# Optimization experiments

Measured on AMD Instinct MI355X. Metric: run time of the kernel, lower is better.

Reference implementation:

```python
import jax, jax.numpy as jnp
import numpy as np

RADIUS = 0.2
NSAMPLE = 64


def _ball_query(xyz, new_xyz):
    """PointNet++-style ball query: first NSAMPLE point indices within RADIUS
    of each center; empty slots filled with the first found index.
    xyz: (B, N, 3), new_xyz: (B, P, 3) -> idx: (B, P, NSAMPLE) int32."""
    N = xyz.shape[1]
    # squared distances (B, P, N)
    d2 = jnp.sum((new_xyz[:, :, None, :] - xyz[:, None, :, :]) ** 2, axis=-1)
    # score = point index if inside ball else sentinel N; smallest NSAMPLE scores
    # give the first NSAMPLE in-ball indices in ascending order (CUDA order).
    scores = jnp.where(d2 < RADIUS * RADIUS, jnp.arange(N, dtype=jnp.int32), N)
    neg_vals, _ = jax.lax.top_k(-scores, NSAMPLE)
    idx = -neg_vals  # ascending smallest scores
    first = idx[..., :1]
    return jnp.where(idx < N, idx, first)


def setup_inputs() -> dict:
    key = jax.random.key(0)
    k1, k2, k3 = jax.random.split(key, 3)
    B, N, P, C = 4, 16384, 1024, 128
    xyz = jax.random.uniform(k1, (B, N, 3), dtype=jnp.float32)
    new_xyz = jax.random.uniform(k2, (B, P, 3), dtype=jnp.float32)
    features = jax.random.normal(k3, (B, C, N), dtype=jnp.float32)
    return {"xyz": xyz, "new_xyz": new_xyz, "features": features}


def reference(xyz, new_xyz, features):
    B, N, _ = xyz.shape
    idx0 = _ball_query(xyz, new_xyz)  # (B, P, S), returned as bq_idx
    # dedup: slots (other than slot 0) equal to the first index are the
    # padding fills -> redirect them to the shadow point at index N
    first = idx0[..., :1]
    dup = (idx0 == first).at[..., 0].set(False)
    idx = jnp.where(dup, N, idx0)

    # shadow xyz = 1e6, shadow feature = 0
    xyz_pad = jnp.concatenate([xyz, jnp.full((B, 1, 3), 1.0e6, xyz.dtype)], axis=1)
    grouped_xyz = jax.vmap(lambda p, i: p[i])(xyz_pad, idx)        # (B, P, S, 3)
    grouped_xyz = grouped_xyz.transpose(0, 3, 1, 2)                # (B, 3, P, S)
    grouped_xyz = grouped_xyz - new_xyz.transpose(0, 2, 1)[..., None]

    feats_pad = jnp.concatenate([features, jnp.zeros_like(features[:, :, :1])], axis=-1)
    grouped_feat = jax.vmap(lambda p, i: p[i])(feats_pad.transpose(0, 2, 1), idx)  # (B, P, S, C)
    grouped_feat = grouped_feat.transpose(0, 3, 1, 2)              # (B, C, P, S)

    # use_xyz=True: zero shadow coords, normalize by radius, concat
    xyz_feature = jnp.where(grouped_xyz > 1.0e5, 0.0, grouped_xyz) / RADIUS
    new_features = jnp.concatenate([xyz_feature, grouped_feat], axis=1)  # (B, 3+C, P, S)
    return new_features, grouped_xyz, idx0
```

## Files before the change

kernel.cpp:

```cpp
#include <hip/hip_runtime.h>
#include <cstdint>

#define BQ_B 4
#define BQ_N 16384
#define BQ_P 1024
#define BQ_C 128
#define NS   64
#define R2   0.04f

#define O1 ((size_t)BQ_B * 131 * BQ_P * NS)
#define O2 (O1 + (size_t)BQ_B * 3 * BQ_P * NS)

#define WS_T_BYTES ((size_t)BQ_B * BQ_N * BQ_C * 4)

__global__ __launch_bounds__(256) void transpose_kernel(
    const float* __restrict__ f, float* __restrict__ ft)
{
    const int bid = blockIdx.x;
    const int n0 = (bid & 255) * 64;
    const int c0 = ((bid >> 8) & 1) * 64;
    const int b  = bid >> 9;
    __shared__ float tile[64][65];

    const float* fb = f + ((size_t)b * BQ_C + c0) * BQ_N;
    #pragma unroll
    for (int k = 0; k < 16; ++k) {
        const int cc = k * 4 + (threadIdx.x >> 6);
        const int nn = threadIdx.x & 63;
        tile[cc][nn] = fb[(size_t)cc * BQ_N + n0 + nn];
    }
    __syncthreads();
    float* ob = ft + ((size_t)b * BQ_N + n0) * BQ_C + c0;
    #pragma unroll
    for (int k = 0; k < 16; ++k) {
        const int nn = k * 4 + (threadIdx.x >> 6);
        const int cc = threadIdx.x & 63;
        ob[(size_t)nn * BQ_C + cc] = tile[cc][nn];
    }
}

__global__ __launch_bounds__(512, 8) void query_gather_kernel(
    const float* __restrict__ xyz,
    const float* __restrict__ new_xyz,
    const float* __restrict__ ft,
    float* __restrict__ out)
{
#pragma clang fp contract(off)
    const int center = blockIdx.x;
    const int b = center >> 10;
    const int p = center & (BQ_P - 1);
    const int t = threadIdx.x;
    const int lane = t & 63;
    const int w = t >> 6;

    __shared__ unsigned long long smask[64];
    __shared__ int   sprefix[64];
    __shared__ int   s_total;
    __shared__ int   lds_idx[NS];
    __shared__ int   gidx_s[NS];
    __shared__ float tile[NS][BQ_C + 1];

    const float cx = new_xyz[center * 3 + 0];
    const float cy = new_xyz[center * 3 + 1];
    const float cz = new_xyz[center * 3 + 2];
    const float* xb = xyz + (size_t)b * BQ_N * 3;

    int total = 0;
    const unsigned long long lmask = (1ull << lane) - 1ull;

    for (int round = 0; round < 4; ++round) {
        const int rbase = round * 4096;
        #pragma unroll
        for (int k = 0; k < 8; ++k) {
            const int j = w * 8 + k;
            const int i = rbase + j * 64 + lane;
            const float dx = xb[i * 3 + 0] - cx;
            const float dy = xb[i * 3 + 1] - cy;
            const float dz = xb[i * 3 + 2] - cz;
            const float d2 = dx * dx + dy * dy + dz * dz;
            const unsigned long long m = __ballot(d2 < R2);
            if (lane == 0) smask[j] = m;
        }
        __syncthreads();

        if (w == 0) {
            const unsigned long long mm = smask[lane];
            const int cnt = (int)__popcll(mm);
            int x = cnt;
            #pragma unroll
            for (int d = 1; d < 64; d <<= 1) {
                const int y = __shfl_up(x, d, 64);
                if (lane >= d) x += y;
            }
            sprefix[lane] = total + (x - cnt);
            if (lane == 63) s_total = total + x;
        }
        __syncthreads();

        const int new_total = s_total;
        #pragma unroll
        for (int k = 0; k < 8; ++k) {
            const int j = w * 8 + k;
            const unsigned long long m = smask[j];
            const int baser = sprefix[j];
            if (baser < NS && ((m >> lane) & 1ull)) {
                const int r = baser + (int)__popcll(m & lmask);
                if (r < NS) lds_idx[r] = rbase + j * 64 + lane;
            }
        }
        total = new_total;
        if (new_total >= NS) break;
    }
    __syncthreads();

    if (t < NS) {
        const int tt = (total > NS) ? NS : total;
        const int first = (total > 0) ? lds_idx[0] : BQ_N;
        const int v = (t < tt) ? lds_idx[t] : BQ_N;
        const int idx0 = (t < tt) ? v : first;
        const int gidx = v;
        const bool real = gidx < BQ_N;
        gidx_s[t] = gidx;

        out[O2 + (size_t)center * NS + t] = (float)idx0;

        #pragma unroll
        for (int d = 0; d < 3; ++d) {
            const float c = (d == 0) ? cx : ((d == 1) ? cy : cz);
            const float pt = real ? xb[gidx * 3 + d] : 1000000.0f;
            const float g = pt - c;
            out[O1 + ((size_t)(b * 3 + d) * BQ_P + p) * NS + t] = g;
            const float xf = ((g > 100000.0f) ? 0.0f : g) / 0.2f;
            out[((size_t)(b * 131 + d) * BQ_P + p) * NS + t] = xf;
        }
    }
    __syncthreads();

    const float* fb = ft + (size_t)b * BQ_N * BQ_C;
    #pragma unroll
    for (int k = 0; k < 16; ++k) {
        const int s = k * 4 + (t >> 7);
        const int c = t & 127;
        const int gi = gidx_s[s];
        tile[s][c] = (gi < BQ_N) ? fb[(size_t)gi * BQ_C + c] : 0.0f;
    }
    __syncthreads();
    float* ob = out + ((size_t)(b * 131 + 3) * BQ_P + p) * NS;
    #pragma unroll
    for (int k = 0; k < 16; ++k) {
        const int c = k * 8 + (t >> 6);
        const int s = t & 63;
        ob[(size_t)c * (BQ_P * NS) + s] = tile[s][c];
    }
}

extern "C" void kernel_launch(void* const* d_in, const int* in_sizes, int n_in,
                              void* d_out, int out_size, void* d_ws, size_t ws_size,
                              hipStream_t stream) {
    const float* xyz      = (const float*)d_in[0];
    const float* new_xyz  = (const float*)d_in[1];
    const float* features = (const float*)d_in[2];
    float* out = (float*)d_out;
    float* ft  = (float*)d_ws;

    transpose_kernel<<<dim3(BQ_B * 2 * 256), dim3(256), 0, stream>>>(features, ft);
    query_gather_kernel<<<dim3(BQ_B * BQ_P), dim3(512), 0, stream>>>(xyz, new_xyz, ft, out);
}
```

Baseline: 234.6 us.

## Split ball query and feature gather into separate kernels with float4 gather

Splits the fused query+gather kernel into a ball-query kernel, which writes indices to workspace, and a separate row-gather kernel. The query block shrinks from 512 to 256 threads, with each wave scanning 16 chunks. The gather kernel uses float4 loads from the transposed features and float4 stores to the output. The aim is to free the heavy-LDS gather from the scan's occupancy limits and to vectorize memory access. The cost is an extra launch and an index round trip through global memory, and LDS column reads in the float4 store may hit bank conflicts.

```diff
diff --git a/kernel.cpp b/kernel.cpp
--- a/kernel.cpp
+++ b/kernel.cpp
@@ -39,10 +39,10 @@
     }
 }
 
-__global__ __launch_bounds__(512, 8) void query_gather_kernel(
+__global__ __launch_bounds__(256) void ballquery_kernel(
     const float* __restrict__ xyz,
     const float* __restrict__ new_xyz,
-    const float* __restrict__ ft,
+    int* __restrict__ wsIdx,
     float* __restrict__ out)
 {
 #pragma clang fp contract(off)
@@ -54,11 +54,9 @@
     const int w = t >> 6;
 
     __shared__ unsigned long long smask[64];
-    __shared__ int   sprefix[64];
-    __shared__ int   s_total;
-    __shared__ int   lds_idx[NS];
-    __shared__ int   gidx_s[NS];
-    __shared__ float tile[NS][BQ_C + 1];
+    __shared__ int sprefix[64];
+    __shared__ int s_total;
+    __shared__ int lds_idx[NS];
 
     const float cx = new_xyz[center * 3 + 0];
     const float cy = new_xyz[center * 3 + 1];
@@ -71,8 +69,8 @@
     for (int round = 0; round < 4; ++round) {
         const int rbase = round * 4096;
         #pragma unroll
-        for (int k = 0; k < 8; ++k) {
-            const int j = w * 8 + k;
+        for (int k = 0; k < 16; ++k) {
+            const int j = w * 16 + k;
             const int i = rbase + j * 64 + lane;
             const float dx = xb[i * 3 + 0] - cx;
             const float dy = xb[i * 3 + 1] - cy;
@@ -99,8 +97,8 @@
 
         const int new_total = s_total;
         #pragma unroll
-        for (int k = 0; k < 8; ++k) {
-            const int j = w * 8 + k;
+        for (int k = 0; k < 16; ++k) {
+            const int j = w * 16 + k;
             const unsigned long long m = smask[j];
             const int baser = sprefix[j];
             if (baser < NS && ((m >> lane) & 1ull)) {
@@ -118,39 +116,61 @@
         const int first = (total > 0) ? lds_idx[0] : BQ_N;
         const int v = (t < tt) ? lds_idx[t] : BQ_N;
         const int idx0 = (t < tt) ? v : first;
-        const int gidx = v;
-        const bool real = gidx < BQ_N;
-        gidx_s[t] = gidx;
+        const bool real = v < BQ_N;
 
+        wsIdx[(size_t)center * NS + t] = v;
         out[O2 + (size_t)center * NS + t] = (float)idx0;
 
         #pragma unroll
         for (int d = 0; d < 3; ++d) {
             const float c = (d == 0) ? cx : ((d == 1) ? cy : cz);
-            const float pt = real ? xb[gidx * 3 + d] : 1000000.0f;
+            const float pt = real ? xb[v * 3 + d] : 1000000.0f;
             const float g = pt - c;
             out[O1 + ((size_t)(b * 3 + d) * BQ_P + p) * NS + t] = g;
             const float xf = ((g > 100000.0f) ? 0.0f : g) / 0.2f;
             out[((size_t)(b * 131 + d) * BQ_P + p) * NS + t] = xf;
         }
     }
+}
+
+__global__ __launch_bounds__(256) void row_gather_kernel(
+    const float* __restrict__ ft,
+    const int* __restrict__ wsIdx,
+    float* __restrict__ out)
+{
+    const int center = blockIdx.x;
+    const int b = center >> 10;
+    const int p = center & (BQ_P - 1);
+    const int t = threadIdx.x;
+
+    __shared__ int   sg[NS];
+    __shared__ float tile[NS][BQ_C + 1];
+
+    if (t < NS) sg[t] = wsIdx[(size_t)center * NS + t];
     __syncthreads();
 
     const float* fb = ft + (size_t)b * BQ_N * BQ_C;
     #pragma unroll
-    for (int k = 0; k < 16; ++k) {
-        const int s = k * 4 + (t >> 7);
-        const int c = t & 127;
-        const int gi = gidx_s[s];
-        tile[s][c] = (gi < BQ_N) ? fb[(size_t)gi * BQ_C + c] : 0.0f;
+    for (int k = 0; k < 8; ++k) {
+        const int s  = k * 8 + (t >> 5);
+        const int c4 = (t & 31) * 4;
+        const int gi = sg[s];
+        float4 v = make_float4(0.f, 0.f, 0.f, 0.f);
+        if (gi < BQ_N) v = *(const float4*)(fb + (size_t)gi * BQ_C + c4);
+        tile[s][c4 + 0] = v.x;
+        tile[s][c4 + 1] = v.y;
+        tile[s][c4 + 2] = v.z;
+        tile[s][c4 + 3] = v.w;
     }
     __syncthreads();
-    float* ob = out + ((size_t)(b * 131 + 3) * BQ_P + p) * NS;
+    float* op = out + ((size_t)(b * 131 + 3) * BQ_P + p) * NS;
     #pragma unroll
-    for (int k = 0; k < 16; ++k) {
-        const int c = k * 8 + (t >> 6);
-        const int s = t & 63;
-        ob[(size_t)c * (BQ_P * NS) + s] = tile[s][c];
+    for (int k = 0; k < 8; ++k) {
+        const int c  = k * 16 + (t >> 4);
+        const int s4 = (t & 15) * 4;
+        float4 v = make_float4(tile[s4 + 0][c], tile[s4 + 1][c],
+                               tile[s4 + 2][c], tile[s4 + 3][c]);
+        *(float4*)(op + (size_t)c * (BQ_P * NS) + s4) = v;
     }
 }
 
@@ -161,8 +181,10 @@
     const float* new_xyz  = (const float*)d_in[1];
     const float* features = (const float*)d_in[2];
     float* out = (float*)d_out;
-    float* ft  = (float*)d_ws;
+    float* ft    = (float*)d_ws;
+    int*   wsIdx = (int*)((char*)d_ws + WS_T_BYTES);
 
     transpose_kernel<<<dim3(BQ_B * 2 * 256), dim3(256), 0, stream>>>(features, ft);
-    query_gather_kernel<<<dim3(BQ_B * BQ_P), dim3(512), 0, stream>>>(xyz, new_xyz, ft, out);
+    ballquery_kernel<<<dim3(BQ_B * BQ_P), dim3(256), 0, stream>>>(xyz, new_xyz, wsIdx, out);
+    row_gather_kernel<<<dim3(BQ_B * BQ_P), dim3(256), 0, stream>>>(ft, wsIdx, out);
 }
```

After: 227.9 us. -2.9%, faster.
